# Performance work log

Hardware: AMD Instinct MI355X
Metric: run time of the kernel (lower is better)

## Reference

```python
import jax, jax.numpy as jnp
import numpy as np

PARENTS = [-1, 0, 0, 0, 1, 2, 3, 4, 5, 6, 7, 8, 9, 9, 9, 12, 13, 14, 16, 17, 18, 19]
NUM_JOINTS = 22
EPS = 1e-12  # matches F.normalize eps


def _cont6d_to_mat(d6):
    """6D rotation rep -> 3x3 rotation matrix (columns b1,b2,b3)."""
    a1, a2 = d6[..., :3], d6[..., 3:]
    b1 = a1 / jnp.maximum(jnp.linalg.norm(a1, axis=-1, keepdims=True), EPS)
    b2 = a2 - b1 * jnp.sum(b1 * a2, axis=-1, keepdims=True)
    b2 = b2 / jnp.maximum(jnp.linalg.norm(b2, axis=-1, keepdims=True), EPS)
    b3 = jnp.cross(b1, b2)
    return jnp.stack((b1, b2, b3), axis=-1)  # [..., 3, 3]


def setup_inputs() -> dict:
    key = jax.random.key(0)
    k1, k2, k3 = jax.random.split(key, 3)
    B, S = 32, 4096
    pred_pos = jax.random.normal(k1, (B, S, 20, 3), dtype=jnp.float32)
    gt_rot = jax.random.normal(k2, (B, S, NUM_JOINTS, 6), dtype=jnp.float32)
    offsets = jax.random.normal(k3, (NUM_JOINTS, 3), dtype=jnp.float32) * 0.2
    return {"pred_pos": pred_pos, "gt_rot": gt_rot, "offsets": offsets}


def reference(pred_pos, gt_rot, offsets):
    B, S = gt_rot.shape[:2]
    dtype = gt_rot.dtype
    rot_mats = _cont6d_to_mat(gt_rot)  # [B,S,22,3,3]
    eye = jnp.broadcast_to(jnp.eye(3, dtype=dtype), (B, S, 3, 3))

    g_rot = [None] * NUM_JOINTS
    g_pos = [None] * NUM_JOINTS
    # Root and joint 1 rotations forced to identity (canonical frame).
    g_rot[0] = eye
    g_pos[0] = jnp.zeros((B, S, 3), dtype=dtype)
    # Sequential FK chain over the fixed 22-joint tree.
    for i in range(1, NUM_JOINTS):
        p = PARENTS[i]
        local_rot = eye if i == 1 else rot_mats[:, :, i]
        g_rot[i] = jnp.einsum('bsij,bsjk->bsik', g_rot[p], local_rot)
        g_pos[i] = g_pos[p] + jnp.einsum('bsij,j->bsi', g_rot[p], offsets[i])

    gt_pos = jnp.stack(g_pos[2:NUM_JOINTS], axis=2)  # [B,S,20,3]
    dist = jnp.linalg.norm(pred_pos - gt_pos, axis=-1)  # [B,S,20]
    mpjpe_mm = dist.mean() * 1000.0
    return mpjpe_mm
```

## Files before the change

### kernel.cpp

```cpp
#include <hip/hip_runtime.h>

#define NJ 22

__device__ __forceinline__ void rot6d_to_mat(float a1x, float a1y, float a1z,
                                             float a2x, float a2y, float a2z,
                                             float* R) {
    float n1 = sqrtf(a1x * a1x + a1y * a1y + a1z * a1z);
    float inv1 = 1.0f / fmaxf(n1, 1e-12f);
    float b1x = a1x * inv1, b1y = a1y * inv1, b1z = a1z * inv1;
    float d = b1x * a2x + b1y * a2y + b1z * a2z;
    float b2x = a2x - b1x * d, b2y = a2y - b1y * d, b2z = a2z - b1z * d;
    float n2 = sqrtf(b2x * b2x + b2y * b2y + b2z * b2z);
    float inv2 = 1.0f / fmaxf(n2, 1e-12f);
    b2x *= inv2; b2y *= inv2; b2z *= inv2;
    float b3x = b1y * b2z - b1z * b2y;
    float b3y = b1z * b2x - b1x * b2z;
    float b3z = b1x * b2y - b1y * b2x;
    R[0] = b1x; R[1] = b2x; R[2] = b3x;
    R[3] = b1y; R[4] = b2y; R[5] = b3y;
    R[6] = b1z; R[7] = b2z; R[8] = b3z;
}

__device__ __forceinline__ void matmul3(const float* __restrict__ A,
                                        const float* __restrict__ B,
                                        float* __restrict__ C) {
#pragma unroll
    for (int r = 0; r < 3; ++r) {
#pragma unroll
        for (int c = 0; c < 3; ++c) {
            C[r * 3 + c] = A[r * 3 + 0] * B[0 * 3 + c]
                         + A[r * 3 + 1] * B[1 * 3 + c]
                         + A[r * 3 + 2] * B[2 * 3 + c];
        }
    }
}

__global__ __launch_bounds__(256) void mpjpe_fk_kernel(
    const float* __restrict__ pred_pos,
    const float* __restrict__ gt_rot,
    const float* __restrict__ offsets,
    float* __restrict__ out,
    int nposes, float scale)
{
    constexpr int PAR[NJ] = {-1, 0, 0, 0, 1, 2, 3, 4, 5, 6, 7, 8, 9, 9, 9, 12, 13, 14, 16, 17, 18, 19};

    int t = blockIdx.x * blockDim.x + threadIdx.x;
    float sum = 0.0f;

    if (t < nposes) {
        const float* gr = gt_rot + (size_t)t * (NJ * 6);
        const float* pp = pred_pos + (size_t)t * (20 * 3);

        float R[NJ][9];
        float P[NJ][3];

        R[0][0] = 1.f; R[0][1] = 0.f; R[0][2] = 0.f;
        R[0][3] = 0.f; R[0][4] = 1.f; R[0][5] = 0.f;
        R[0][6] = 0.f; R[0][7] = 0.f; R[0][8] = 1.f;
        P[0][0] = 0.f; P[0][1] = 0.f; P[0][2] = 0.f;

#pragma unroll
        for (int i = 1; i < NJ; ++i) {
            const int p = PAR[i];
            float ox = offsets[i * 3 + 0];
            float oy = offsets[i * 3 + 1];
            float oz = offsets[i * 3 + 2];
#pragma unroll
            for (int r = 0; r < 3; ++r) {
                P[i][r] = P[p][r] + R[p][r * 3 + 0] * ox
                                  + R[p][r * 3 + 1] * oy
                                  + R[p][r * 3 + 2] * oz;
            }
            if (i == 1) {
#pragma unroll
                for (int k = 0; k < 9; ++k) R[i][k] = R[p][k];
            } else {
                const float2* g2 = (const float2*)(gr + i * 6);
                float2 v0 = g2[0], v1 = g2[1], v2 = g2[2];
                float M[9];
                rot6d_to_mat(v0.x, v0.y, v1.x, v1.y, v2.x, v2.y, M);
                matmul3(R[p], M, R[i]);
            }
            if (i >= 2) {
                float dx = pp[(i - 2) * 3 + 0] - P[i][0];
                float dy = pp[(i - 2) * 3 + 1] - P[i][1];
                float dz = pp[(i - 2) * 3 + 2] - P[i][2];
                sum += sqrtf(dx * dx + dy * dy + dz * dz);
            }
        }
    }

#pragma unroll
    for (int o = 32; o > 0; o >>= 1) sum += __shfl_down(sum, o, 64);

    __shared__ float ws[4];
    int lane = threadIdx.x & 63;
    int wid = threadIdx.x >> 6;
    if (lane == 0) ws[wid] = sum;
    __syncthreads();
    if (threadIdx.x == 0) {
        float s = ws[0] + ws[1] + ws[2] + ws[3];
        atomicAdd(out, s * scale);
    }
}

extern "C" void kernel_launch(void* const* d_in, const int* in_sizes, int n_in,
                              void* d_out, int out_size, void* d_ws, size_t ws_size,
                              hipStream_t stream) {
    const float* pred_pos = (const float*)d_in[0];
    const float* gt_rot   = (const float*)d_in[1];
    const float* offsets  = (const float*)d_in[2];
    float* out = (float*)d_out;

    int nposes = in_sizes[1] / (NJ * 6);
    float scale = 1000.0f / ((float)nposes * 20.0f);

    hipMemsetAsync(out, 0, sizeof(float), stream);

    int block = 256;
    int grid = (nposes + block - 1) / block;
    mpjpe_fk_kernel<<<grid, block, 0, stream>>>(pred_pos, gt_rot, offsets, out, nposes, scale);
}
```

Before: 140.0 us.

## Split FK tree into per-wave chain roles across five waves per pose

Each block now handles 64 poses with 5 wavefronts, and each wavefront walks one kinematic chain of the skeleton using compile-time step tables. This shortens the per-thread serial dependency chain and reduces register pressure, exposing more parallelism for latency hiding. The cost is redundant recomputation of shared ancestor joints (3, 6, 9) in two roles, uneven work between roles, and per-wave access patterns that touch the same pose rows from several waves.

Measured after the change: 145.0 us. 3.6% more time.

```diff
diff --git a/kernel.cpp b/kernel.cpp
--- a/kernel.cpp
+++ b/kernel.cpp
@@ -35,72 +35,100 @@
     }
 }
 
-__global__ __launch_bounds__(256) void mpjpe_fk_kernel(
+struct Step { int j; int reset; int emit; int upR; };
+
+template<int ROLE> struct RoleDef;
+template<> struct RoleDef<0> {
+    static constexpr int NS = 6;
+    static constexpr Step S[6] = {{2,1,1,0},{3,1,1,0},{1,1,0,0},{4,0,1,1},{7,0,1,1},{10,0,1,0}};
+};
+template<> struct RoleDef<1> {
+    static constexpr int NS = 4;
+    static constexpr Step S[4] = {{2,1,0,1},{5,0,1,1},{8,0,1,1},{11,0,1,0}};
+};
+template<> struct RoleDef<2> {
+    static constexpr int NS = 5;
+    static constexpr Step S[5] = {{3,1,0,1},{6,0,1,1},{9,0,1,1},{12,0,1,1},{15,0,1,0}};
+};
+template<> struct RoleDef<3> {
+    static constexpr int NS = 7;
+    static constexpr Step S[7] = {{3,1,0,1},{6,0,0,1},{9,0,0,1},{13,0,1,1},{16,0,1,1},{18,0,1,1},{20,0,1,0}};
+};
+template<> struct RoleDef<4> {
+    static constexpr int NS = 7;
+    static constexpr Step S[7] = {{3,1,0,1},{6,0,0,1},{9,0,0,1},{14,0,1,1},{17,0,1,1},{19,0,1,1},{21,0,1,0}};
+};
+
+template<int ROLE>
+__device__ __forceinline__ float walk(const float* __restrict__ gr,
+                                      const float* __restrict__ pp,
+                                      const float* __restrict__ off) {
+    float R[9] = {1.f,0.f,0.f, 0.f,1.f,0.f, 0.f,0.f,1.f};
+    float P[3] = {0.f,0.f,0.f};
+    float sum = 0.f;
+#pragma unroll
+    for (int s = 0; s < RoleDef<ROLE>::NS; ++s) {
+        const int j = RoleDef<ROLE>::S[s].j;
+        if (RoleDef<ROLE>::S[s].reset) {
+            R[0]=1.f;R[1]=0.f;R[2]=0.f;R[3]=0.f;R[4]=1.f;R[5]=0.f;R[6]=0.f;R[7]=0.f;R[8]=1.f;
+            P[0]=0.f;P[1]=0.f;P[2]=0.f;
+        }
+        float ox = off[j*3+0], oy = off[j*3+1], oz = off[j*3+2];
+        float nx = P[0] + R[0]*ox + R[1]*oy + R[2]*oz;
+        float ny = P[1] + R[3]*ox + R[4]*oy + R[5]*oz;
+        float nz = P[2] + R[6]*ox + R[7]*oy + R[8]*oz;
+        P[0]=nx; P[1]=ny; P[2]=nz;
+        if (RoleDef<ROLE>::S[s].emit) {
+            const float* q = pp + (j-2)*3;
+            float dx = q[0]-nx, dy = q[1]-ny, dz = q[2]-nz;
+            sum += sqrtf(dx*dx + dy*dy + dz*dz);
+        }
+        if (RoleDef<ROLE>::S[s].upR) {
+            const float2* g2 = (const float2*)(gr + j*6);
+            float2 v0 = g2[0], v1 = g2[1], v2 = g2[2];
+            float M[9];
+            rot6d_to_mat(v0.x, v0.y, v1.x, v1.y, v2.x, v2.y, M);
+            float T[9];
+            matmul3(R, M, T);
+#pragma unroll
+            for (int k = 0; k < 9; ++k) R[k] = T[k];
+        }
+    }
+    return sum;
+}
+
+__global__ __launch_bounds__(320) void mpjpe_fk_kernel(
     const float* __restrict__ pred_pos,
     const float* __restrict__ gt_rot,
     const float* __restrict__ offsets,
     float* __restrict__ out,
     int nposes, float scale)
 {
-    constexpr int PAR[NJ] = {-1, 0, 0, 0, 1, 2, 3, 4, 5, 6, 7, 8, 9, 9, 9, 12, 13, 14, 16, 17, 18, 19};
+    const int lane = threadIdx.x & 63;
+    const int wid  = threadIdx.x >> 6;
+    const int pose = blockIdx.x * 64 + lane;
 
-    int t = blockIdx.x * blockDim.x + threadIdx.x;
-    float sum = 0.0f;
-
-    if (t < nposes) {
-        const float* gr = gt_rot + (size_t)t * (NJ * 6);
-        const float* pp = pred_pos + (size_t)t * (20 * 3);
-
-        float R[NJ][9];
-        float P[NJ][3];
-
-        R[0][0] = 1.f; R[0][1] = 0.f; R[0][2] = 0.f;
-        R[0][3] = 0.f; R[0][4] = 1.f; R[0][5] = 0.f;
-        R[0][6] = 0.f; R[0][7] = 0.f; R[0][8] = 1.f;
-        P[0][0] = 0.f; P[0][1] = 0.f; P[0][2] = 0.f;
-
-#pragma unroll
-        for (int i = 1; i < NJ; ++i) {
-            const int p = PAR[i];
-            float ox = offsets[i * 3 + 0];
-            float oy = offsets[i * 3 + 1];
-            float oz = offsets[i * 3 + 2];
-#pragma unroll
-            for (int r = 0; r < 3; ++r) {
-                P[i][r] = P[p][r] + R[p][r * 3 + 0] * ox
-                                  + R[p][r * 3 + 1] * oy
-                                  + R[p][r * 3 + 2] * oz;
-            }
-            if (i == 1) {
-#pragma unroll
-                for (int k = 0; k < 9; ++k) R[i][k] = R[p][k];
-            } else {
-                const float2* g2 = (const float2*)(gr + i * 6);
-                float2 v0 = g2[0], v1 = g2[1], v2 = g2[2];
-                float M[9];
-                rot6d_to_mat(v0.x, v0.y, v1.x, v1.y, v2.x, v2.y, M);
-                matmul3(R[p], M, R[i]);
-            }
-            if (i >= 2) {
-                float dx = pp[(i - 2) * 3 + 0] - P[i][0];
-                float dy = pp[(i - 2) * 3 + 1] - P[i][1];
-                float dz = pp[(i - 2) * 3 + 2] - P[i][2];
-                sum += sqrtf(dx * dx + dy * dy + dz * dz);
-            }
+    float sum = 0.f;
+    if (pose < nposes) {
+        const float* gr = gt_rot  + (size_t)pose * (NJ * 6);
+        const float* pp = pred_pos + (size_t)pose * (20 * 3);
+        switch (wid) {
+            case 0: sum = walk<0>(gr, pp, offsets); break;
+            case 1: sum = walk<1>(gr, pp, offsets); break;
+            case 2: sum = walk<2>(gr, pp, offsets); break;
+            case 3: sum = walk<3>(gr, pp, offsets); break;
+            case 4: sum = walk<4>(gr, pp, offsets); break;
         }
     }
 
 #pragma unroll
     for (int o = 32; o > 0; o >>= 1) sum += __shfl_down(sum, o, 64);
 
-    __shared__ float ws[4];
-    int lane = threadIdx.x & 63;
-    int wid = threadIdx.x >> 6;
+    __shared__ float ws[5];
     if (lane == 0) ws[wid] = sum;
     __syncthreads();
     if (threadIdx.x == 0) {
-        float s = ws[0] + ws[1] + ws[2] + ws[3];
-        atomicAdd(out, s * scale);
+        atomicAdd(out, (ws[0] + ws[1] + ws[2] + ws[3] + ws[4]) * scale);
     }
 }
 
@@ -117,7 +145,7 @@
 
     hipMemsetAsync(out, 0, sizeof(float), stream);
 
-    int block = 256;
-    int grid = (nposes + block - 1) / block;
+    int block = 320;
+    int grid = (nposes + 63) / 64;
     mpjpe_fk_kernel<<<grid, block, 0, stream>>>(pred_pos, gt_rot, offsets, out, nposes, scale);
 }
```
